# Performance work log

Measured on AMD Instinct MI355X. Metric: run time of the kernel, lower is better.

Reference implementation:

```python
import jax, jax.numpy as jnp
import numpy as np

B, S, D = 2, 2048, 2048
Q_HEADS, KV_HEADS = 16, 4
D_HEAD = D // Q_HEADS            # 128
GROUPS = Q_HEADS // KV_HEADS     # 4
SCALE = D_HEAD ** -0.5
ROPE_THETA = 10000.0


def apply_rope(x, cos, sin):
    # x: (b, h, s, dh); cos/sin: (s, dh//2) -> rotate interleaved pairs
    xp = x.reshape(*x.shape[:-1], D_HEAD // 2, 2)
    xr, xi = xp[..., 0], xp[..., 1]
    c = cos[None, None, :, :]
    s = sin[None, None, :, :]
    outr = xr * c - xi * s
    outi = xr * s + xi * c
    return jnp.stack([outr, outi], axis=-1).reshape(x.shape)


def setup_inputs() -> dict:
    key = jax.random.key(0)
    ks = jax.random.split(key, 10)
    x = jax.random.normal(ks[0], (B, S, D), dtype=jnp.float32)
    # RoPE angles: pos * inv_freq, shape (S, D_HEAD//2)
    inv_freq = 1.0 / (ROPE_THETA ** (jnp.arange(0, D_HEAD, 2, dtype=jnp.float32) / D_HEAD))
    rope_freq = jnp.arange(S, dtype=jnp.float32)[:, None] * inv_freq[None, :]
    # causal additive mask (1,1,S,S)
    causal = jnp.tril(jnp.ones((S, S), dtype=bool))
    mask = jnp.where(causal, 0.0, -1e9).astype(jnp.float32)[None, None]
    std = D ** -0.5
    wq_w = jax.random.normal(ks[1], (Q_HEADS * D_HEAD, D), dtype=jnp.float32) * std
    wq_b = jnp.zeros((Q_HEADS * D_HEAD,), dtype=jnp.float32)
    wk_w = jax.random.normal(ks[2], (KV_HEADS * D_HEAD, D), dtype=jnp.float32) * std
    wk_b = jnp.zeros((KV_HEADS * D_HEAD,), dtype=jnp.float32)
    wv_w = jax.random.normal(ks[3], (KV_HEADS * D_HEAD, D), dtype=jnp.float32) * std
    wv_b = jnp.zeros((KV_HEADS * D_HEAD,), dtype=jnp.float32)
    wo_w = jax.random.normal(ks[4], (D, Q_HEADS * D_HEAD), dtype=jnp.float32) * std
    wo_b = jnp.zeros((D,), dtype=jnp.float32)
    return {"x": x, "rope_freq": rope_freq, "mask": mask,
            "wq_w": wq_w, "wq_b": wq_b, "wk_w": wk_w, "wk_b": wk_b,
            "wv_w": wv_w, "wv_b": wv_b, "wo_w": wo_w, "wo_b": wo_b}


def reference(x, rope_freq, mask, wq_w, wq_b, wk_w, wk_b, wv_w, wv_b, wo_w, wo_b):
    b, s, d = x.shape
    cos, sin = jnp.cos(rope_freq), jnp.sin(rope_freq)
    # projections (torch Linear: y = x @ W^T + b)
    q = (x @ wq_w.T + wq_b).reshape(b, s, Q_HEADS, D_HEAD).transpose(0, 2, 1, 3)
    k = (x @ wk_w.T + wk_b).reshape(b, s, KV_HEADS, D_HEAD).transpose(0, 2, 1, 3)
    v = (x @ wv_w.T + wv_b).reshape(b, s, KV_HEADS, D_HEAD).transpose(0, 2, 1, 3)
    q = apply_rope(q, cos, sin)
    k = apply_rope(k, cos, sin)
    # GQA: repeat_interleave KV heads to match query heads
    k = jnp.repeat(k, GROUPS, axis=1)  # (b, Q_HEADS, s, dh)
    v = jnp.repeat(v, GROUPS, axis=1)
    scores = jnp.einsum('bhqd,bhkd->bhqk', q, k)
    scores = (scores + mask) * SCALE  # faithful: mask added BEFORE scaling
    attn = jax.nn.softmax(scores, axis=-1)
    out = jnp.einsum('bhqk,bhkd->bhqd', attn, v)
    out = out.transpose(0, 2, 1, 3).reshape(b, s, d)
    return out @ wo_w.T + wo_b
```

## Files before the change

kernel.cpp:

```cpp
#include <hip/hip_runtime.h>
#include <hip/hip_bf16.h>
#include <stdint.h>

typedef float floatx4 __attribute__((ext_vector_type(4)));
typedef __bf16 bfx8 __attribute__((ext_vector_type(8)));

#define ATT_SCALE 0.08838834764831845f

__device__ __forceinline__ uint16_t f2bf(float f) {
  uint32_t u = __float_as_uint(f);
  return (uint16_t)((u + 0x7fffu + ((u >> 16) & 1u)) >> 16);
}
__device__ __forceinline__ float bf2f(uint32_t bits16) {
  return __uint_as_float(bits16 << 16);
}

typedef __attribute__((address_space(3))) uint32_t lds_u32;
typedef const __attribute__((address_space(1))) uint32_t glob_u32;

__device__ __forceinline__ void async_copy16(void* lds, const void* g) {
  uint32_t loff = (uint32_t)(uintptr_t)lds;
  loff = (uint32_t)__builtin_amdgcn_readfirstlane((int)loff);
  lds_u32* lp = reinterpret_cast<lds_u32*>(loff);
  glob_u32* gp = reinterpret_cast<glob_u32*>((uintptr_t)g);
  __builtin_amdgcn_global_load_lds(gp, lp, 16, 0, 0);
}

__global__ void cvt5_kernel(const float* __restrict__ x,  const float* __restrict__ wq,
                            const float* __restrict__ wk, const float* __restrict__ wv,
                            const float* __restrict__ wo,
                            uint16_t* __restrict__ xb,  uint16_t* __restrict__ wqb,
                            uint16_t* __restrict__ wkb, uint16_t* __restrict__ wvb,
                            uint16_t* __restrict__ wob) {
  const int bid = blockIdx.x;
  const float* src; uint16_t* dst; int base;
  if (bid < 8192)       { src = x;  dst = xb;  base = 0; }
  else if (bid < 12288) { src = wq; dst = wqb; base = 8192; }
  else if (bid < 13312) { src = wk; dst = wkb; base = 12288; }
  else if (bid < 14336) { src = wv; dst = wvb; base = 13312; }
  else                  { src = wo; dst = wob; base = 14336; }
  const int i = (((bid - base) << 8) + threadIdx.x) << 2;
  const float4 v = *(const float4*)(src + i);
  uint32_t lo = (uint32_t)f2bf(v.x) | ((uint32_t)f2bf(v.y) << 16);
  uint32_t hi = (uint32_t)f2bf(v.z) | ((uint32_t)f2bf(v.w) << 16);
  *(uint2*)(dst + i) = make_uint2(lo, hi);
}

__global__ void rope2_kernel(uint32_t* __restrict__ qb, uint32_t* __restrict__ kb,
                             const float* __restrict__ freq) {
  const int bid = blockIdx.x;
  uint32_t* buf; int idx, shift; float post;
  if (bid < 16384) { buf = qb; idx = (bid << 8) + threadIdx.x; shift = 10; post = ATT_SCALE; }
  else { buf = kb; idx = ((bid - 16384) << 8) + threadIdx.x; shift = 8; post = 1.0f; }
  const int row = idx >> shift;
  const int cp  = idx & ((1 << shift) - 1);
  const int s = row & 2047;
  const int f = cp & 63;
  const float fr = freq[(s << 6) + f];
  float sn, c;
  sincosf(fr, &sn, &c);
  const uint32_t u = buf[idx];
  const float xr = bf2f(u & 0xffffu);
  const float xi = bf2f(u >> 16);
  const float orr = (xr * c - xi * sn) * post;
  const float oi  = (xr * sn + xi * c) * post;
  buf[idx] = (uint32_t)f2bf(orr) | ((uint32_t)f2bf(oi) << 16);
}

template <int BM, int MODE>
__global__ __launch_bounds__(512, 2) void gemm3(
    const uint16_t* __restrict__ A,
    const uint16_t* __restrict__ Wq, const uint16_t* __restrict__ Wk,
    const uint16_t* __restrict__ Wv,
    const float* __restrict__ bq, const float* __restrict__ bk,
    const float* __restrict__ bv,
    uint16_t* __restrict__ Qo, uint16_t* __restrict__ Ko,
    uint16_t* __restrict__ Vt, float* __restrict__ Fo) {
  constexpr int NT  = 64;
  constexpr int MR  = BM / 32;
  constexpr int NLW = BM / 128 + 2;

  const int tid  = threadIdx.x;
  const int w    = tid >> 6;
  const int lane = tid & 63;
  const int l15  = lane & 15;
  const int l4   = lane >> 4;
  const int wr   = w >> 2;
  const int wc   = w & 3;
  const int bm = blockIdx.x * BM;
  const int n0 = blockIdx.y * 256;

  const uint16_t* Wp;
  int wrow;
  if constexpr (MODE == 0) {
    if (n0 < 2048)      { Wp = Wq; wrow = n0; }
    else if (n0 < 2560) { Wp = Wk; wrow = n0 - 2048; }
    else                { Wp = Wv; wrow = n0 - 2560; }
  } else {
    Wp = Wq; wrow = n0;
  }

  __shared__ uint16_t As[3][BM * 32];
  __shared__ uint16_t Bs[3][256 * 32];

  floatx4 acc[MR][4] = {};

  const int srow = lane >> 2;
  const int sg   = lane & 3;

  auto stageA = [&](int buf, int t) {
#pragma unroll
    for (int i = 0; i < BM / 128; ++i) {
      const int r0i = w * (BM / 8) + i * 16;
      const int r = r0i + srow;
      const char* src = (const char*)A +
          ((size_t)(bm + r) * 2048 + t * 32) * 2 + ((sg ^ (r & 3)) << 4);
      async_copy16((char*)(As[buf]) + r0i * 64, src);
    }
  };
  auto stageB = [&](int buf, int t) {
#pragma unroll
    for (int i = 0; i < 2; ++i) {
      const int r0i = w * 32 + i * 16;
      const int r = r0i + srow;
      const char* src = (const char*)Wp +
          ((size_t)(wrow + r) * 2048 + t * 32) * 2 + ((sg ^ (r & 3)) << 4);
      async_copy16((char*)(Bs[buf]) + r0i * 64, src);
    }
  };

  stageA(0, 0); stageB(0, 0);
  stageA(1, 1); stageB(1, 1);
  asm volatile("s_waitcnt vmcnt(%0)" :: "i"(NLW) : "memory");
  __builtin_amdgcn_s_barrier();

  int c0 = 0;
  for (int t = 0; t < NT; ++t) {
    const char* AsB = (const char*)(As[c0]);
    const char* BsB = (const char*)(Bs[c0]);

    bfx8 bf_[4], af_[MR];
#pragma unroll
    for (int n = 0; n < 4; ++n) {
      const int r = wc * 64 + n * 16 + l15;
      bf_[n] = *(const bfx8*)(BsB + r * 64 + ((l4 ^ (r & 3)) << 4));
    }
#pragma unroll
    for (int m = 0; m < MR; ++m) {
      const int r = wr * (BM / 2) + m * 16 + l15;
      af_[m] = *(const bfx8*)(AsB + r * 64 + ((l4 ^ (r & 3)) << 4));
    }

    int c2 = c0 + 2; if (c2 >= 3) c2 -= 3;
    if (t + 2 < NT) { stageA(c2, t + 2); stageB(c2, t + 2); }

    asm volatile("s_waitcnt lgkmcnt(0)" ::: "memory");
    __builtin_amdgcn_sched_barrier(0);
    __builtin_amdgcn_s_setprio(1);
#pragma unroll
    for (int m = 0; m < MR; ++m)
#pragma unroll
      for (int n = 0; n < 4; ++n)
        acc[m][n] = __builtin_amdgcn_mfma_f32_16x16x32_bf16(af_[m], bf_[n], acc[m][n], 0, 0, 0);
    __builtin_amdgcn_s_setprio(0);

    if (t + 2 < NT)      asm volatile("s_waitcnt vmcnt(%0)" :: "i"(NLW) : "memory");
    else if (t + 1 < NT) asm volatile("s_waitcnt vmcnt(0)" ::: "memory");
    if (t + 1 < NT) __builtin_amdgcn_s_barrier();
    if (++c0 == 3) c0 = 0;
  }

  const int rb = bm + wr * (BM / 2) + (l4 << 2);
  const int cl = wc * 64 + l15;
#pragma unroll
  for (int n = 0; n < 4; ++n) {
    const int c = n0 + cl + (n << 4);
#pragma unroll
    for (int m = 0; m < MR; ++m) {
      const int r0 = rb + (m << 4);
      if constexpr (MODE == 1) {
        const float bias = bq[c];
#pragma unroll
        for (int j = 0; j < 4; ++j)
          Fo[(size_t)(r0 + j) * 2048 + c] = acc[m][n][j] + bias;
      } else {
        if (n0 < 2048) {
          const float bias = bq[c];
#pragma unroll
          for (int j = 0; j < 4; ++j)
            Qo[(size_t)(r0 + j) * 2048 + c] = f2bf(acc[m][n][j] + bias);
        } else if (n0 < 2560) {
          const int ck = c - 2048;
          const float bias = bk[ck];
#pragma unroll
          for (int j = 0; j < 4; ++j)
            Ko[(size_t)(r0 + j) * 512 + ck] = f2bf(acc[m][n][j] + bias);
        } else {
          const int cv = c - 2560;
          const float bias = bv[cv];
          const int b = r0 >> 11, s = r0 & 2047;
          const int kv = cv >> 7, dh = cv & 127;
          uint32_t lo = (uint32_t)f2bf(acc[m][n][0] + bias) | ((uint32_t)f2bf(acc[m][n][1] + bias) << 16);
          uint32_t hi = (uint32_t)f2bf(acc[m][n][2] + bias) | ((uint32_t)f2bf(acc[m][n][3] + bias) << 16);
          *(uint2*)(Vt + (size_t)(((b << 2) + kv) * 128 + dh) * 2048 + s) = make_uint2(lo, hi);
        }
      }
    }
  }
}

__global__ __launch_bounds__(256) void attn_kernel(
    const uint16_t* __restrict__ Q, const uint16_t* __restrict__ Kb,
    const uint16_t* __restrict__ Vt, uint16_t* __restrict__ O) {
  const int px  = blockIdx.x;
  const int h   = blockIdx.y;
  const int b   = blockIdx.z;
  const int kvh = h >> 2;
  const int tid  = threadIdx.x;
  const int w    = tid >> 6;
  const int lane = tid & 63;
  const int l15 = lane & 15;
  const int l4  = lane >> 4;

  __shared__ uint16_t Ks[2][64 * 128];
  __shared__ uint16_t Vs[2][128 * 64];
  __shared__ uint16_t Ps[4][16 * 64];
  char* PsB = (char*)(Ps[w]);

  const int krow_off = l4;
  const int kscb = l15 << 4;
  const int vrow_off = lane >> 3;
  const int vscb = (lane & 7) << 4;

  auto stageK = [&](int buf, int t) {
    const int kb = t << 6;
#pragma unroll
    for (int i = 0; i < 4; ++i) {
      const int base_r = 16 * w + 4 * i;
      const int r = base_r + krow_off;
      const int scb = kscb ^ ((r & 7) << 4);
      const char* src = (const char*)Kb + ((size_t)(b * 2048 + kb + r) * 512 + kvh * 128) * 2 + scb;
      async_copy16((char*)(Ks[buf]) + base_r * 256, src);
    }
  };
  auto stageV = [&](int buf, int t) {
    const int kb = t << 6;
#pragma unroll
    for (int i = 0; i < 4; ++i) {
      const int base_r = 32 * w + 8 * i;
      const int r = base_r + vrow_off;
      const int scb = vscb ^ ((r & 7) << 4);
      const char* src = (const char*)Vt + ((size_t)(((b << 2) + kvh) * 128 + r) * 2048 + kb) * 2 + scb;
      async_copy16((char*)(Vs[buf]) + base_r * 128, src);
    }
  };

  for (int half = 0; half < 2; ++half) {
    const int qt = half ? (31 - px) : px;
    const int qbase = qt << 6;

    bfx8 qf[4];
    {
      const size_t qrow = (size_t)(b * 2048 + qbase + (w << 4) + l15);
      const char* qp = (const char*)(Q + qrow * 2048 + h * 128 + l4 * 8);
#pragma unroll
      for (int kk = 0; kk < 4; ++kk) qf[kk] = *(const bfx8*)(qp + kk * 64);
    }

    floatx4 oacc[8] = {};
    float mrun[4], lrun[4];
#pragma unroll
    for (int j = 0; j < 4; ++j) { mrun[j] = -1e30f; lrun[j] = 0.0f; }

    stageK(0, 0);
    stageV(0, 0);
    __syncthreads();

    for (int t = 0; t <= qt; ++t) {
      const int cur = t & 1;
      if (t < qt) { stageK(cur ^ 1, t + 1); stageV(cur ^ 1, t + 1); }
      char* KsB = (char*)(Ks[cur]);
      char* VsB = (char*)(Vs[cur]);
      const int kb = t << 6;

      floatx4 sc[4] = {};
      __builtin_amdgcn_s_setprio(1);
#pragma unroll
      for (int kk = 0; kk < 4; ++kk) {
        const int cb = (kk << 6) + (l4 << 4);
#pragma unroll
        for (int n = 0; n < 4; ++n) {
          const int r = (n << 4) + l15;
          bfx8 kf = *(const bfx8*)(KsB + r * 256 + (cb ^ ((r & 7) << 4)));
          sc[n] = __builtin_amdgcn_mfma_f32_16x16x32_bf16(qf[kk], kf, sc[n], 0, 0, 0);
        }
      }
      __builtin_amdgcn_s_setprio(0);

      float p[4][4];
      const bool diag = (t == qt);
#pragma unroll
      for (int n = 0; n < 4; ++n) {
#pragma unroll
        for (int j = 0; j < 4; ++j) {
          float v = sc[n][j];
          if (diag) {
            const int col = kb + (n << 4) + l15;
            const int row = qbase + (w << 4) + (l4 << 2) + j;
            if (col > row) v = -1e30f;
          }
          p[n][j] = v;
        }
      }

#pragma unroll
      for (int j = 0; j < 4; ++j) {
        float pm = fmaxf(fmaxf(p[0][j], p[1][j]), fmaxf(p[2][j], p[3][j]));
#pragma unroll
        for (int off = 8; off > 0; off >>= 1) pm = fmaxf(pm, __shfl_xor(pm, off, 64));
        const float mnew = fmaxf(mrun[j], pm);
        const float sf = __expf(mrun[j] - mnew);
        mrun[j] = mnew;
        float rs = 0.f;
#pragma unroll
        for (int n = 0; n < 4; ++n) {
          p[n][j] = __expf(p[n][j] - mnew);
          rs += p[n][j];
        }
        lrun[j] = lrun[j] * sf + rs;
#pragma unroll
        for (int d = 0; d < 8; ++d) oacc[d][j] *= sf;
      }

#pragma unroll
      for (int n = 0; n < 4; ++n) {
        const int cbw = (n << 5) + (l15 << 1);
#pragma unroll
        for (int j = 0; j < 4; ++j) {
          const int r = (l4 << 2) + j;
          *(uint16_t*)(PsB + r * 128 + (cbw ^ ((r & 7) << 4))) = f2bf(p[n][j]);
        }
      }

      __builtin_amdgcn_s_setprio(1);
#pragma unroll
      for (int kk = 0; kk < 2; ++kk) {
        const int cb = (kk << 6) + (l4 << 4);
        bfx8 pf = *(const bfx8*)(PsB + l15 * 128 + (cb ^ ((l15 & 7) << 4)));
#pragma unroll
        for (int d = 0; d < 8; ++d) {
          const int r = (d << 4) + l15;
          bfx8 vf = *(const bfx8*)(VsB + r * 128 + (cb ^ ((r & 7) << 4)));
          oacc[d] = __builtin_amdgcn_mfma_f32_16x16x32_bf16(pf, vf, oacc[d], 0, 0, 0);
        }
      }
      __builtin_amdgcn_s_setprio(0);

      __syncthreads();
    }

#pragma unroll
    for (int j = 0; j < 4; ++j) {
      float l = lrun[j];
#pragma unroll
      for (int off = 8; off > 0; off >>= 1) l += __shfl_xor(l, off, 64);
      const float inv = 1.0f / l;
      const size_t row = (size_t)(b * 2048 + qbase + (w << 4) + (l4 << 2) + j);
#pragma unroll
      for (int d = 0; d < 8; ++d) {
        const int c = h * 128 + (d << 4) + l15;
        O[row * 2048 + c] = f2bf(oacc[d][j] * inv);
      }
    }
  }
}

extern "C" void kernel_launch(void* const* d_in, const int* in_sizes, int n_in,
                              void* d_out, int out_size, void* d_ws, size_t ws_size,
                              hipStream_t stream) {
  (void)in_sizes; (void)n_in; (void)out_size; (void)ws_size;
  const float* x         = (const float*)d_in[0];
  const float* rope_freq = (const float*)d_in[1];
  const float* wq_w = (const float*)d_in[3];
  const float* wq_b = (const float*)d_in[4];
  const float* wk_w = (const float*)d_in[5];
  const float* wk_b = (const float*)d_in[6];
  const float* wv_w = (const float*)d_in[7];
  const float* wv_b = (const float*)d_in[8];
  const float* wo_w = (const float*)d_in[9];
  const float* wo_b = (const float*)d_in[10];
  float* out = (float*)d_out;

  char* ws = (char*)d_ws;
  uint16_t* xbf = (uint16_t*)(ws + 0);
  uint16_t* wqb = (uint16_t*)(ws + 16777216);
  uint16_t* wkb = (uint16_t*)(ws + 25165824);
  uint16_t* wvb = (uint16_t*)(ws + 27262976);
  uint16_t* wob = (uint16_t*)(ws + 29360128);
  uint16_t* qbf = (uint16_t*)(ws + 37748736);
  uint16_t* kbf = (uint16_t*)(ws + 54525952);
  uint16_t* vtb = (uint16_t*)(ws + 58720256);
  uint16_t* att = (uint16_t*)(ws + 62914560);

  cvt5_kernel<<<18432, 256, 0, stream>>>(x, wq_w, wk_w, wv_w, wo_w,
                                         xbf, wqb, wkb, wvb, wob);

  gemm3<256, 0><<<dim3(16, 12), 512, 0, stream>>>(
      xbf, wqb, wkb, wvb, wq_b, wk_b, wv_b, qbf, kbf, vtb, nullptr);

  rope2_kernel<<<20480, 256, 0, stream>>>((uint32_t*)qbf, (uint32_t*)kbf, rope_freq);

  attn_kernel<<<dim3(16, 16, 2), 256, 0, stream>>>(qbf, kbf, vtb, att);

  gemm3<128, 1><<<dim3(32, 8), 512, 0, stream>>>(
      att, wob, nullptr, nullptr, wo_b, nullptr, nullptr,
      nullptr, nullptr, nullptr, out);
}
```

Measured before the change: 335.7 us.

## Use 128x128 GEMM tiles and 128-row query tiles with 8-wave attention blocks

Replaces the 256-wide, 512-thread GEMM with a 128x128, 256-thread variant so the QKV and output projections launch more blocks (768 and 512), aiming at better CU occupancy on the many-CU GPU. The attention kernel now uses 8 waves per block, each covering 128 query rows, so every K/V tile staged in LDS is shared by twice as many waves, and the causal diagonal now spans two KV tiles. In exchange, each GEMM tile reuses less data and the attention grid shrinks to 256 blocks, which may lower parallelism.

```diff
diff --git a/kernel.cpp b/kernel.cpp
--- a/kernel.cpp
+++ b/kernel.cpp
@@ -67,8 +67,8 @@
   buf[idx] = (uint32_t)f2bf(orr) | ((uint32_t)f2bf(oi) << 16);
 }
 
-template <int BM, int MODE>
-__global__ __launch_bounds__(512, 2) void gemm3(
+template <int MODE>
+__global__ __launch_bounds__(256, 3) void gemm4(
     const uint16_t* __restrict__ A,
     const uint16_t* __restrict__ Wq, const uint16_t* __restrict__ Wk,
     const uint16_t* __restrict__ Wv,
@@ -76,19 +76,17 @@
     const float* __restrict__ bv,
     uint16_t* __restrict__ Qo, uint16_t* __restrict__ Ko,
     uint16_t* __restrict__ Vt, float* __restrict__ Fo) {
-  constexpr int NT  = 64;
-  constexpr int MR  = BM / 32;
-  constexpr int NLW = BM / 128 + 2;
+  constexpr int NT = 64;
 
   const int tid  = threadIdx.x;
   const int w    = tid >> 6;
   const int lane = tid & 63;
   const int l15  = lane & 15;
   const int l4   = lane >> 4;
-  const int wr   = w >> 2;
-  const int wc   = w & 3;
-  const int bm = blockIdx.x * BM;
-  const int n0 = blockIdx.y * 256;
+  const int wr   = w >> 1;
+  const int wc   = w & 1;
+  const int bm = blockIdx.x << 7;
+  const int n0 = blockIdx.y << 7;
 
   const uint16_t* Wp;
   int wrow;
@@ -100,38 +98,31 @@
     Wp = Wq; wrow = n0;
   }
 
-  __shared__ uint16_t As[3][BM * 32];
-  __shared__ uint16_t Bs[3][256 * 32];
-
-  floatx4 acc[MR][4] = {};
+  __shared__ uint16_t As[3][128 * 32];
+  __shared__ uint16_t Bs[3][128 * 32];
+
+  floatx4 acc[4][4] = {};
 
   const int srow = lane >> 2;
   const int sg   = lane & 3;
 
-  auto stageA = [&](int buf, int t) {
-#pragma unroll
-    for (int i = 0; i < BM / 128; ++i) {
-      const int r0i = w * (BM / 8) + i * 16;
+  auto stage = [&](int buf, int t) {
+#pragma unroll
+    for (int i = 0; i < 2; ++i) {
+      const int r0i = (w << 5) + (i << 4);
       const int r = r0i + srow;
-      const char* src = (const char*)A +
+      const char* srcA = (const char*)A +
           ((size_t)(bm + r) * 2048 + t * 32) * 2 + ((sg ^ (r & 3)) << 4);
-      async_copy16((char*)(As[buf]) + r0i * 64, src);
+      async_copy16((char*)(As[buf]) + r0i * 64, srcA);
+      const char* srcB = (const char*)Wp +
+          ((size_t)(wrow + r) * 2048 + t * 32) * 2 + ((sg ^ (r & 3)) << 4);
+      async_copy16((char*)(Bs[buf]) + r0i * 64, srcB);
     }
   };
-  auto stageB = [&](int buf, int t) {
-#pragma unroll
-    for (int i = 0; i < 2; ++i) {
-      const int r0i = w * 32 + i * 16;
-      const int r = r0i + srow;
-      const char* src = (const char*)Wp +
-          ((size_t)(wrow + r) * 2048 + t * 32) * 2 + ((sg ^ (r & 3)) << 4);
-      async_copy16((char*)(Bs[buf]) + r0i * 64, src);
-    }
-  };
-
-  stageA(0, 0); stageB(0, 0);
-  stageA(1, 1); stageB(1, 1);
-  asm volatile("s_waitcnt vmcnt(%0)" :: "i"(NLW) : "memory");
+
+  stage(0, 0);
+  stage(1, 1);
+  asm volatile("s_waitcnt vmcnt(4)" ::: "memory");
   __builtin_amdgcn_s_barrier();
 
   int c0 = 0;
@@ -139,44 +130,44 @@
     const char* AsB = (const char*)(As[c0]);
     const char* BsB = (const char*)(Bs[c0]);
 
-    bfx8 bf_[4], af_[MR];
+    bfx8 af_[4], bf_[4];
 #pragma unroll
     for (int n = 0; n < 4; ++n) {
-      const int r = wc * 64 + n * 16 + l15;
+      const int r = (wc << 6) + (n << 4) + l15;
       bf_[n] = *(const bfx8*)(BsB + r * 64 + ((l4 ^ (r & 3)) << 4));
     }
 #pragma unroll
-    for (int m = 0; m < MR; ++m) {
-      const int r = wr * (BM / 2) + m * 16 + l15;
+    for (int m = 0; m < 4; ++m) {
+      const int r = (wr << 6) + (m << 4) + l15;
       af_[m] = *(const bfx8*)(AsB + r * 64 + ((l4 ^ (r & 3)) << 4));
     }
 
     int c2 = c0 + 2; if (c2 >= 3) c2 -= 3;
-    if (t + 2 < NT) { stageA(c2, t + 2); stageB(c2, t + 2); }
+    if (t + 2 < NT) stage(c2, t + 2);
 
     asm volatile("s_waitcnt lgkmcnt(0)" ::: "memory");
     __builtin_amdgcn_sched_barrier(0);
     __builtin_amdgcn_s_setprio(1);
 #pragma unroll
-    for (int m = 0; m < MR; ++m)
+    for (int m = 0; m < 4; ++m)
 #pragma unroll
       for (int n = 0; n < 4; ++n)
         acc[m][n] = __builtin_amdgcn_mfma_f32_16x16x32_bf16(af_[m], bf_[n], acc[m][n], 0, 0, 0);
     __builtin_amdgcn_s_setprio(0);
 
-    if (t + 2 < NT)      asm volatile("s_waitcnt vmcnt(%0)" :: "i"(NLW) : "memory");
+    if (t + 2 < NT)      asm volatile("s_waitcnt vmcnt(4)" ::: "memory");
     else if (t + 1 < NT) asm volatile("s_waitcnt vmcnt(0)" ::: "memory");
     if (t + 1 < NT) __builtin_amdgcn_s_barrier();
     if (++c0 == 3) c0 = 0;
   }
 
-  const int rb = bm + wr * (BM / 2) + (l4 << 2);
-  const int cl = wc * 64 + l15;
+  const int rb = bm + (wr << 6) + (l4 << 2);
+  const int cl = (wc << 6) + l15;
 #pragma unroll
   for (int n = 0; n < 4; ++n) {
     const int c = n0 + cl + (n << 4);
 #pragma unroll
-    for (int m = 0; m < MR; ++m) {
+    for (int m = 0; m < 4; ++m) {
       const int r0 = rb + (m << 4);
       if constexpr (MODE == 1) {
         const float bias = bq[c];
@@ -209,7 +200,7 @@
   }
 }
 
-__global__ __launch_bounds__(256) void attn_kernel(
+__global__ __launch_bounds__(512, 4) void attn_kernel(
     const uint16_t* __restrict__ Q, const uint16_t* __restrict__ Kb,
     const uint16_t* __restrict__ Vt, uint16_t* __restrict__ O) {
   const int px  = blockIdx.x;
@@ -224,7 +215,7 @@
 
   __shared__ uint16_t Ks[2][64 * 128];
   __shared__ uint16_t Vs[2][128 * 64];
-  __shared__ uint16_t Ps[4][16 * 64];
+  __shared__ uint16_t Ps[8][16 * 64];
   char* PsB = (char*)(Ps[w]);
 
   const int krow_off = l4;
@@ -235,8 +226,8 @@
   auto stageK = [&](int buf, int t) {
     const int kb = t << 6;
 #pragma unroll
-    for (int i = 0; i < 4; ++i) {
-      const int base_r = 16 * w + 4 * i;
+    for (int i = 0; i < 2; ++i) {
+      const int base_r = (w << 3) + (i << 2);
       const int r = base_r + krow_off;
       const int scb = kscb ^ ((r & 7) << 4);
       const char* src = (const char*)Kb + ((size_t)(b * 2048 + kb + r) * 512 + kvh * 128) * 2 + scb;
@@ -246,8 +237,8 @@
   auto stageV = [&](int buf, int t) {
     const int kb = t << 6;
 #pragma unroll
-    for (int i = 0; i < 4; ++i) {
-      const int base_r = 32 * w + 8 * i;
+    for (int i = 0; i < 2; ++i) {
+      const int base_r = (w << 4) + (i << 3);
       const int r = base_r + vrow_off;
       const int scb = vscb ^ ((r & 7) << 4);
       const char* src = (const char*)Vt + ((size_t)(((b << 2) + kvh) * 128 + r) * 2048 + kb) * 2 + scb;
@@ -256,8 +247,9 @@
   };
 
   for (int half = 0; half < 2; ++half) {
-    const int qt = half ? (31 - px) : px;
-    const int qbase = qt << 6;
+    const int qt = half ? (15 - px) : px;
+    const int qbase = qt << 7;
+    const int nt = (qt << 1) + 2;
 
     bfx8 qf[4];
     {
@@ -276,9 +268,9 @@
     stageV(0, 0);
     __syncthreads();
 
-    for (int t = 0; t <= qt; ++t) {
+    for (int t = 0; t < nt; ++t) {
       const int cur = t & 1;
-      if (t < qt) { stageK(cur ^ 1, t + 1); stageV(cur ^ 1, t + 1); }
+      if (t + 1 < nt) { stageK(cur ^ 1, t + 1); stageV(cur ^ 1, t + 1); }
       char* KsB = (char*)(Ks[cur]);
       char* VsB = (char*)(Vs[cur]);
       const int kb = t << 6;
@@ -298,7 +290,7 @@
       __builtin_amdgcn_s_setprio(0);
 
       float p[4][4];
-      const bool diag = (t == qt);
+      const bool diag = (t >= (qt << 1));
 #pragma unroll
       for (int n = 0; n < 4; ++n) {
 #pragma unroll
@@ -405,14 +397,14 @@
   cvt5_kernel<<<18432, 256, 0, stream>>>(x, wq_w, wk_w, wv_w, wo_w,
                                          xbf, wqb, wkb, wvb, wob);
 
-  gemm3<256, 0><<<dim3(16, 12), 512, 0, stream>>>(
+  gemm4<0><<<dim3(32, 24), 256, 0, stream>>>(
       xbf, wqb, wkb, wvb, wq_b, wk_b, wv_b, qbf, kbf, vtb, nullptr);
 
   rope2_kernel<<<20480, 256, 0, stream>>>((uint32_t*)qbf, (uint32_t*)kbf, rope_freq);
 
-  attn_kernel<<<dim3(16, 16, 2), 256, 0, stream>>>(qbf, kbf, vtb, att);
-
-  gemm3<128, 1><<<dim3(32, 8), 512, 0, stream>>>(
+  attn_kernel<<<dim3(8, 16, 2), 512, 0, stream>>>(qbf, kbf, vtb, att);
+
+  gemm4<1><<<dim3(32, 16), 256, 0, stream>>>(
       att, wob, nullptr, nullptr, wo_b, nullptr, nullptr,
       nullptr, nullptr, nullptr, out);
 }
```

After: 345.3 us. +2.9%, slower.
